# Optimization experiments

Hardware: AMD Instinct MI355X
Metric: run time of the kernel (lower is better)

The kernel has to match this reference:

```python
import jax, jax.numpy as jnp
import numpy as np

DIM_SINGLE = 384
DIM_PAIR = 128
HEADS = 12
DIM_POINT = 4
B, N = 1, 1024
EPS = 1e-5


def _gram_schmidt_rot(key, shape):
    k1, k2 = jax.random.split(key)
    v1 = jax.random.normal(k1, shape + (3,), jnp.float32)
    v2 = jax.random.normal(k2, shape + (3,), jnp.float32)
    x = v1 / jnp.linalg.norm(v1, axis=-1, keepdims=True)
    z = jnp.cross(x, v2)
    z = z / jnp.linalg.norm(z, axis=-1, keepdims=True)
    y = jnp.cross(z, x)
    # columns are basis vectors, matching torch.stack([x,y,z], dim=-1)
    return jnp.stack([x, y, z], axis=-1)


def setup_inputs() -> dict:
    key = jax.random.key(0)
    ks = jax.random.split(key, 24)
    C, Cp, H, P = DIM_SINGLE, DIM_PAIR, HEADS, DIM_POINT
    HP3 = H * P * 3
    s = lambda k, sh, sc: (jax.random.normal(k, sh, jnp.float32) * sc)
    inp = {
        'single': jax.random.normal(ks[0], (B, N, C), jnp.float32),
        'pair': jax.random.normal(ks[1], (B, N, N, Cp), jnp.float32),
        'rot': _gram_schmidt_rot(ks[2], (B, N)),
        'trans': jax.random.normal(ks[3], (B, N, 3), jnp.float32),
        'mask': jnp.ones((B, N), dtype=bool),
        'Wq': s(ks[4], (C, C), C ** -0.5), 'bq': jnp.zeros((C,), jnp.float32),
        'Wk': s(ks[5], (C, C), C ** -0.5), 'bk': jnp.zeros((C,), jnp.float32),
        'Wv': s(ks[6], (C, C), C ** -0.5), 'bv': jnp.zeros((C,), jnp.float32),
        'Wpb': s(ks[7], (Cp, H), Cp ** -0.5), 'bpb': jnp.zeros((H,), jnp.float32),
        'Wqp': s(ks[8], (C, HP3), C ** -0.5), 'bqp': jnp.zeros((HP3,), jnp.float32),
        'Wkp': s(ks[9], (C, HP3), C ** -0.5), 'bkp': jnp.zeros((HP3,), jnp.float32),
        'Wvp': s(ks[10], (C, HP3), C ** -0.5), 'bvp': jnp.zeros((HP3,), jnp.float32),
        'Wo': s(ks[11], (C, C), C ** -0.5), 'bo': jnp.zeros((C,), jnp.float32),
        'Wpo': s(ks[12], (HP3, C), HP3 ** -0.5), 'bpo': jnp.zeros((C,), jnp.float32),
        'gamma': jnp.ones((C,), jnp.float32), 'beta': jnp.zeros((C,), jnp.float32),
    }
    return inp


def ipa_forward(single, pair, rot, trans, mask,
                Wq, bq, Wk, bk, Wv, bv, Wpb, bpb,
                Wqp, bqp, Wkp, bkp, Wvp, bvp,
                Wo, bo, Wpo, bpo, gamma, beta):
    Bn, Nn, C = single.shape
    H, P = HEADS, DIM_POINT
    Ch = C // H
    scale = Ch ** -0.5

    q = (single @ Wq + bq).reshape(Bn, Nn, H, Ch)
    k = (single @ Wk + bk).reshape(Bn, Nn, H, Ch)
    v = (single @ Wv + bv).reshape(Bn, Nn, H, Ch)

    pair_bias = (pair @ Wpb + bpb).transpose(0, 3, 1, 2)  # [B,H,N,N]

    def pts(W, b):
        p = (single @ W + b).reshape(Bn, Nn, H, P, 3)
        # point as row-vector times rot (matches torch einsum bnhpd,bnhde->bnhpe)
        p = jnp.einsum('bnhpd,bnde->bnhpe', p, rot) + trans[:, :, None, None, :]
        return p

    q_pts = pts(Wqp, bqp)
    k_pts = pts(Wkp, bkp)
    v_pts = pts(Wvp, bvp)

    q2 = jnp.sum(q_pts ** 2, axis=(3, 4))  # [B,N,H]
    k2 = jnp.sum(k_pts ** 2, axis=(3, 4))

    scalar_logits = jnp.einsum('bmhc,bnhc->bhmn', q, k) * scale
    qk_pts = jnp.einsum('bmhpd,bnhpd->bhmn', q_pts, k_pts)
    point_logits = -0.5 * (q2.transpose(0, 2, 1)[:, :, :, None]
                           + k2.transpose(0, 2, 1)[:, :, None, :]
                           - 2.0 * qk_pts) * scale
    logits = scalar_logits + point_logits + pair_bias

    mask2d = mask[:, None, :, None] & mask[:, None, None, :]  # [B,1,M,N]
    logits = jnp.where(mask2d, logits, -1e9)

    attn = jax.nn.softmax(logits, axis=-1)  # [B,H,M,N]

    out_scalar = jnp.einsum('bhmn,bnhc->bmhc', attn, v).reshape(Bn, Nn, C)
    out_points = jnp.einsum('bhmn,bnhpd->bmhpd', attn, v_pts).reshape(Bn, Nn, H * P * 3)

    out = out_scalar @ Wo + bo + out_points @ Wpo + bpo
    x = single + out
    mu = jnp.mean(x, axis=-1, keepdims=True)
    var = jnp.var(x, axis=-1, keepdims=True)
    return (x - mu) / jnp.sqrt(var + EPS) * gamma + beta


def reference(single, pair, rot, trans, mask,
              Wq, bq, Wk, bk, Wv, bv, Wpb, bpb,
              Wqp, bqp, Wkp, bkp, Wvp, bvp,
              Wo, bo, Wpo, bpo, gamma, beta):
    return ipa_forward(single, pair, rot, trans, mask,
                       Wq, bq, Wk, bk, Wv, bv, Wpb, bpb,
                       Wqp, bqp, Wkp, bkp, Wvp, bvp,
                       Wo, bo, Wpo, bpo, gamma, beta)
```

## Files before the change

### kernel.cpp

```cpp
#include <hip/hip_runtime.h>
#include <cmath>


#define SCALE 0.17677669529663687f

#define OFF_QQ 0u
#define OFF_KK 589824u
#define OFF_VV 1179648u
#define OFF_SM 1769472u
#define OFF_SIS 1781760u
#define OFF_OA4 1794048u
#define OFF_OA 3956736u
#define OFF_LG 4497408u
#define OFF_TMP 17080320u
#define WS_FLOATS 18702336ull

__device__ __forceinline__ void fma4(float4& a, const float4& w, float s) {
  a.x = fmaf(w.x, s, a.x); a.y = fmaf(w.y, s, a.y);
  a.z = fmaf(w.z, s, a.z); a.w = fmaf(w.w, s, a.w);
}

__global__ __launch_bounds__(256) void k_gemm(
    const float* __restrict__ single,
    const float* __restrict__ Wq, const float* __restrict__ bq,
    const float* __restrict__ Wk, const float* __restrict__ bk,
    const float* __restrict__ Wv, const float* __restrict__ bv,
    const float* __restrict__ Wqp, const float* __restrict__ bqp,
    const float* __restrict__ Wkp, const float* __restrict__ bkp,
    const float* __restrict__ Wvp, const float* __restrict__ bvp,
    float* __restrict__ TMP)
{
  __shared__ float sA[64 * 37];
  __shared__ float sB[48 * 37];
  const int tid = threadIdx.x;
  const int m0 = blockIdx.x * 64;
  const int ct = blockIdx.y;
  const float* W; const float* bb; int OUT, cb;
  if (ct < 24) {
    int w_ = ct >> 3;
    W  = w_ == 0 ? Wq : (w_ == 1 ? Wk : Wv);
    bb = w_ == 0 ? bq : (w_ == 1 ? bk : bv);
    OUT = 384; cb = (ct & 7) * 48;
  } else {
    int pt = ct - 24; int w_ = pt / 3;
    W  = w_ == 0 ? Wqp : (w_ == 1 ? Wkp : Wvp);
    bb = w_ == 0 ? bqp : (w_ == 1 ? bkp : bvp);
    OUT = 144; cb = (pt - w_ * 3) * 48;
  }
  const int tr = tid >> 4, tc = tid & 15;
  const int r0 = tr * 4;
  const int k4s = tid & 7, mrs = tid >> 3;
  const int c4b = tid % 12, kkb = tid / 12;
  const int f1 = tid + 256;
  const int c4b1 = f1 % 12, kkb1 = f1 / 12;

  float acc[4][3];
  #pragma unroll
  for (int i = 0; i < 4; ++i)
    #pragma unroll
    for (int j = 0; j < 3; ++j) acc[i][j] = 0.f;

  float4 pa0 = *(const float4*)&single[(size_t)(m0 + mrs) * 384 + k4s * 4];
  float4 pa1 = *(const float4*)&single[(size_t)(m0 + mrs + 32) * 384 + k4s * 4];
  float4 pb0 = *(const float4*)&W[(size_t)kkb * OUT + cb + c4b * 4];
  float4 pb1;
  if (tid < 128) pb1 = *(const float4*)&W[(size_t)kkb1 * OUT + cb + c4b1 * 4];

  for (int kc = 0; kc < 12; ++kc) {
    *(float4*)&sA[mrs * 37 + k4s * 4] = pa0;
    *(float4*)&sA[(mrs + 32) * 37 + k4s * 4] = pa1;
    sB[(c4b * 4 + 0) * 37 + kkb] = pb0.x;
    sB[(c4b * 4 + 1) * 37 + kkb] = pb0.y;
    sB[(c4b * 4 + 2) * 37 + kkb] = pb0.z;
    sB[(c4b * 4 + 3) * 37 + kkb] = pb0.w;
    if (tid < 128) {
      sB[(c4b1 * 4 + 0) * 37 + kkb1] = pb1.x;
      sB[(c4b1 * 4 + 1) * 37 + kkb1] = pb1.y;
      sB[(c4b1 * 4 + 2) * 37 + kkb1] = pb1.z;
      sB[(c4b1 * 4 + 3) * 37 + kkb1] = pb1.w;
    }
    if (kc < 11) {
      int kn = (kc + 1) * 32;
      pa0 = *(const float4*)&single[(size_t)(m0 + mrs) * 384 + kn + k4s * 4];
      pa1 = *(const float4*)&single[(size_t)(m0 + mrs + 32) * 384 + kn + k4s * 4];
      pb0 = *(const float4*)&W[(size_t)(kn + kkb) * OUT + cb + c4b * 4];
      if (tid < 128) pb1 = *(const float4*)&W[(size_t)(kn + kkb1) * OUT + cb + c4b1 * 4];
    }
    __syncthreads();
    #pragma unroll
    for (int k4 = 0; k4 < 8; ++k4) {
      float4 av[4], bv_[3];
      #pragma unroll
      for (int i = 0; i < 4; ++i) av[i] = *(const float4*)&sA[(r0 + i) * 37 + k4 * 4];
      #pragma unroll
      for (int j = 0; j < 3; ++j) bv_[j] = *(const float4*)&sB[(tc * 3 + j) * 37 + k4 * 4];
      #pragma unroll
      for (int i = 0; i < 4; ++i)
        #pragma unroll
        for (int j = 0; j < 3; ++j)
          acc[i][j] += av[i].x * bv_[j].x + av[i].y * bv_[j].y
                     + av[i].z * bv_[j].z + av[i].w * bv_[j].w;
    }
    __syncthreads();
  }
  #pragma unroll
  for (int i = 0; i < 4; ++i)
    #pragma unroll
    for (int j = 0; j < 3; ++j) {
      int c = tc * 3 + j;
      TMP[(size_t)(m0 + r0 + i) * 1584 + ct * 48 + c] = acc[i][j] + bb[cb + c];
    }
}

__global__ __launch_bounds__(256) void k_epi(
    const float* __restrict__ TMP, const float* __restrict__ rotm,
    const float* __restrict__ trans, const float* __restrict__ bpb,
    float* __restrict__ ws)
{
  __shared__ float srot[288];
  const int tid = threadIdx.x;
  const int m = blockIdx.x;
  const float* t = TMP + (size_t)m * 1584;
  float* QQ = ws + OFF_QQ; float* KK = ws + OFF_KK; float* VV = ws + OFF_VV;

  for (int i = tid; i < 1152; i += 256) {
    int seg = i / 384, idx = i - seg * 384;
    int h = idx >> 5, c = idx & 31;
    float val = t[i];
    if (seg == 0)      QQ[h * 49152 + m * 48 + c] = SCALE * val;
    else if (seg == 1) KK[h * 49152 + m * 48 + c] = val;
    else               VV[m * 576 + h * 48 + c] = val;
  }
  const float* R = rotm + m * 9;
  for (int i = tid; i < 432; i += 256) {
    int seg = i / 144, r = i - seg * 144;
    int h = r / 12, pe = r - h * 12, p = pe / 3, e = pe - p * 3;
    const float* raw = t + 1152 + seg * 144 + h * 12 + p * 3;
    float val = raw[0] * R[e] + raw[1] * R[3 + e] + raw[2] * R[6 + e] + trans[m * 3 + e];
    if (seg == 0)      { srot[r] = val;       QQ[h * 49152 + m * 48 + 32 + pe] = SCALE * val; }
    else if (seg == 1) { srot[144 + r] = val; KK[h * 49152 + m * 48 + 32 + pe] = val; }
    else               VV[m * 576 + h * 48 + 32 + pe] = val;
  }
  __syncthreads();
  if (tid < 24) {
    int seg = tid / 12, h = tid - seg * 12;
    float s2 = 0.f;
    #pragma unroll
    for (int j = 0; j < 12; ++j) {
      float x = srot[seg * 144 + h * 12 + j];
      s2 = fmaf(x, x, s2);
    }
    if (seg == 0) {
      float* d = QQ + h * 49152 + m * 48;
      d[44] = 1.f; d[45] = -0.5f * SCALE * s2; d[46] = 0.f; d[47] = 0.f;
    } else {
      float* d = KK + h * 49152 + m * 48;
      d[44] = bpb[h] - 0.5f * SCALE * s2; d[45] = 1.f; d[46] = 0.f; d[47] = 0.f;
    }
  }
}

__global__ __launch_bounds__(256) void k_qkdot(const float* __restrict__ QQ,
                                               const float* __restrict__ KK,
                                               float* __restrict__ LG)
{
  __shared__ float sQ[64 * 52];
  __shared__ float sK[128 * 52];
  const int tid = threadIdx.x;
  const int n0 = blockIdx.x * 128, m0 = blockIdx.y * 64, hh = blockIdx.z;
  const float* Qg = QQ + (size_t)hh * 49152 + (size_t)m0 * 48;
  const float* Kg = KK + (size_t)hh * 49152 + (size_t)n0 * 48;
  for (int i = tid; i < 768; i += 256) {
    int r = i / 12, c4 = (i - r * 12) * 4;
    *(float4*)&sQ[r * 52 + c4] = *(const float4*)&Qg[r * 48 + c4];
  }
  for (int i = tid; i < 1536; i += 256) {
    int r = i / 12, c4 = (i - r * 12) * 4;
    *(float4*)&sK[r * 52 + c4] = *(const float4*)&Kg[r * 48 + c4];
  }
  __syncthreads();
  const int mb = (tid >> 4) * 4, nb = tid & 15;
  float acc[4][8];
  #pragma unroll
  for (int i = 0; i < 4; ++i)
    #pragma unroll
    for (int j = 0; j < 8; ++j) acc[i][j] = 0.f;
  #pragma unroll
  for (int j4 = 0; j4 < 48; j4 += 4) {
    float4 q[4], k[8];
    #pragma unroll
    for (int i = 0; i < 4; ++i) q[i] = *(const float4*)&sQ[(mb + i) * 52 + j4];
    #pragma unroll
    for (int j = 0; j < 8; ++j) k[j] = *(const float4*)&sK[(nb + j * 16) * 52 + j4];
    #pragma unroll
    for (int i = 0; i < 4; ++i)
      #pragma unroll
      for (int j = 0; j < 8; ++j)
        acc[i][j] += q[i].x * k[j].x + q[i].y * k[j].y + q[i].z * k[j].z + q[i].w * k[j].w;
  }
  float* Lb = LG + (size_t)hh * 1048576 + (size_t)m0 * 1024 + n0;
  #pragma unroll
  for (int i = 0; i < 4; ++i)
    #pragma unroll
    for (int j = 0; j < 8; ++j)
      Lb[(mb + i) * 1024 + nb + j * 16] = acc[i][j];
}

__global__ __launch_bounds__(256) void k_bias(const float* __restrict__ pair,
                                              const float* __restrict__ Wpb,
                                              float* __restrict__ LG)
{
  __shared__ float sP[256 * 33];
  const int tid = threadIdx.x;
  const size_t base = (size_t)blockIdx.x * 256;
  const int c4 = tid & 7, r8 = tid >> 3;
  float acc[12];
  #pragma unroll
  for (int h = 0; h < 12; ++h) acc[h] = 0.f;

  float4 pre[8];
  #pragma unroll
  for (int k = 0; k < 8; ++k)
    pre[k] = *(const float4*)&pair[(base + k * 32 + r8) * 128 + c4 * 4];

  for (int cc = 0; cc < 4; ++cc) {
    #pragma unroll
    for (int k = 0; k < 8; ++k) {
      float* d = &sP[(k * 32 + r8) * 33 + c4 * 4];
      d[0] = pre[k].x; d[1] = pre[k].y; d[2] = pre[k].z; d[3] = pre[k].w;
    }
    if (cc < 3) {
      #pragma unroll
      for (int k = 0; k < 8; ++k)
        pre[k] = *(const float4*)&pair[(base + k * 32 + r8) * 128 + (cc + 1) * 32 + c4 * 4];
    }
    __syncthreads();
    const float* rp = &sP[tid * 33];
    #pragma unroll 8
    for (int j = 0; j < 32; ++j) {
      float p = rp[j];
      const float* w = Wpb + (cc * 32 + j) * 12;
      #pragma unroll
      for (int h = 0; h < 12; ++h) acc[h] = fmaf(p, w[h], acc[h]);
    }
    __syncthreads();
  }
  float* L = LG + base + tid;
  #pragma unroll
  for (int h = 0; h < 12; ++h) L[(size_t)h * 1048576] += acc[h];
}

__global__ __launch_bounds__(256) void k_stats(const float* __restrict__ LG,
                                               float* __restrict__ SM,
                                               float* __restrict__ SIS)
{
  const int tid = threadIdx.x;
  const int m0 = blockIdx.x * 16, hh = blockIdx.y;
  const int lane = tid & 63, wv = tid >> 6;
  const float* Lh = LG + (size_t)hh * 1048576;
  #pragma unroll
  for (int rr = 0; rr < 4; ++rr) {
    int r = m0 + wv * 4 + rr;
    float m = -3.0e38f, s = 0.f;
    #pragma unroll
    for (int ch = 0; ch < 4; ++ch) {
      float4 x = *(const float4*)&Lh[(size_t)r * 1024 + ch * 256 + lane * 4];
      float mx = fmaxf(fmaxf(x.x, x.y), fmaxf(x.z, x.w));
      #pragma unroll
      for (int d = 32; d; d >>= 1) mx = fmaxf(mx, __shfl_xor(mx, d));
      float mn = fmaxf(m, mx);
      float sum = __expf(x.x - mn) + __expf(x.y - mn)
                + __expf(x.z - mn) + __expf(x.w - mn);
      #pragma unroll
      for (int d = 32; d; d >>= 1) sum += __shfl_xor(sum, d);
      s = s * __expf(m - mn) + sum;
      m = mn;
    }
    if (lane == 0) {
      SM[hh * 1024 + r] = m;
      SIS[hh * 1024 + r] = 1.f / s;
    }
  }
}

__global__ __launch_bounds__(256) void k_av(const float* __restrict__ LG,
                                            const float* __restrict__ VV,
                                            const float* __restrict__ SM,
                                            float* __restrict__ OA4)
{
  __shared__ float sA[64 * 68];
  __shared__ float sBt[48 * 68];
  __shared__ float sMl[64];
  const int tid = threadIdx.x;
  const int m0 = blockIdx.x * 64, n0 = blockIdx.y * 256, hh = blockIdx.z;
  const int q = blockIdx.y;
  const float* Lh = LG + (size_t)hh * 1048576;
  const int mi4 = tid >> 4, cj3 = tid & 15;

  if (tid < 64) sMl[tid] = SM[hh * 1024 + m0 + tid];
  for (int i = tid; i < 4 * 68; i += 256) sBt[44 * 68 + i] = 0.f;
  __syncthreads();

  float acc[4][3];
  #pragma unroll
  for (int i = 0; i < 4; ++i)
    #pragma unroll
    for (int j = 0; j < 3; ++j) acc[i][j] = 0.f;

  for (int kc = 0; kc < 4; ++kc) {
    const int nb = n0 + kc * 64;
    #pragma unroll
    for (int t = 0; t < 4; ++t) {
      int idx = tid + t * 256;
      int row = idx >> 4, c4 = idx & 15;
      float4 x = *(const float4*)&Lh[(size_t)(m0 + row) * 1024 + nb + c4 * 4];
      float mrow = sMl[row];
      float4 e;
      e.x = __expf(x.x - mrow); e.y = __expf(x.y - mrow);
      e.z = __expf(x.z - mrow); e.w = __expf(x.w - mrow);
      *(float4*)&sA[row * 68 + c4 * 4] = e;
    }
    for (int idx = tid; idx < 704; idx += 256) {
      int r = idx / 11, c4 = idx - r * 11;
      float4 v = *(const float4*)&VV[(size_t)(nb + r) * 576 + hh * 48 + c4 * 4];
      sBt[(c4 * 4 + 0) * 68 + r] = v.x;
      sBt[(c4 * 4 + 1) * 68 + r] = v.y;
      sBt[(c4 * 4 + 2) * 68 + r] = v.z;
      sBt[(c4 * 4 + 3) * 68 + r] = v.w;
    }
    __syncthreads();
    #pragma unroll 4
    for (int k4 = 0; k4 < 16; ++k4) {
      float4 a0 = *(const float4*)&sA[(mi4 * 4 + 0) * 68 + k4 * 4];
      float4 a1 = *(const float4*)&sA[(mi4 * 4 + 1) * 68 + k4 * 4];
      float4 a2 = *(const float4*)&sA[(mi4 * 4 + 2) * 68 + k4 * 4];
      float4 a3 = *(const float4*)&sA[(mi4 * 4 + 3) * 68 + k4 * 4];
      float4 b0 = *(const float4*)&sBt[(cj3 * 3 + 0) * 68 + k4 * 4];
      float4 b1 = *(const float4*)&sBt[(cj3 * 3 + 1) * 68 + k4 * 4];
      float4 b2 = *(const float4*)&sBt[(cj3 * 3 + 2) * 68 + k4 * 4];
      acc[0][0] += a0.x*b0.x + a0.y*b0.y + a0.z*b0.z + a0.w*b0.w;
      acc[0][1] += a0.x*b1.x + a0.y*b1.y + a0.z*b1.z + a0.w*b1.w;
      acc[0][2] += a0.x*b2.x + a0.y*b2.y + a0.z*b2.z + a0.w*b2.w;
      acc[1][0] += a1.x*b0.x + a1.y*b0.y + a1.z*b0.z + a1.w*b0.w;
      acc[1][1] += a1.x*b1.x + a1.y*b1.y + a1.z*b1.z + a1.w*b1.w;
      acc[1][2] += a1.x*b2.x + a1.y*b2.y + a1.z*b2.z + a1.w*b2.w;
      acc[2][0] += a2.x*b0.x + a2.y*b0.y + a2.z*b0.z + a2.w*b0.w;
      acc[2][1] += a2.x*b1.x + a2.y*b1.y + a2.z*b1.z + a2.w*b1.w;
      acc[2][2] += a2.x*b2.x + a2.y*b2.y + a2.z*b2.z + a2.w*b2.w;
      acc[3][0] += a3.x*b0.x + a3.y*b0.y + a3.z*b0.z + a3.w*b0.w;
      acc[3][1] += a3.x*b1.x + a3.y*b1.y + a3.z*b1.z + a3.w*b1.w;
      acc[3][2] += a3.x*b2.x + a3.y*b2.y + a3.z*b2.z + a3.w*b2.w;
    }
    __syncthreads();
  }
  #pragma unroll
  for (int i = 0; i < 4; ++i)
    #pragma unroll
    for (int j = 0; j < 3; ++j) {
      int c = cj3 * 3 + j;
      if (c < 44)
        OA4[(size_t)q * 540672 + (size_t)(m0 + mi4 * 4 + i) * 528 + hh * 44 + c]
            = acc[i][j];
    }
}

__global__ __launch_bounds__(256) void k_merge(const float* __restrict__ OA4,
                                               const float* __restrict__ SIS,
                                               float* __restrict__ OA)
{
  int idx = blockIdx.x * 256 + threadIdx.x;
  if (idx >= 540672) return;
  int m = idx / 528, c = idx - m * 528;
  int h = c / 44;
  float v = OA4[idx] + OA4[540672 + idx] + OA4[2 * 540672 + idx]
          + OA4[3 * 540672 + idx];
  OA[idx] = v * SIS[h * 1024 + m];
}

__global__ __launch_bounds__(128) void k_final(
    const float* __restrict__ OA, const float* __restrict__ single,
    const float* __restrict__ Wo, const float* __restrict__ bo,
    const float* __restrict__ Wpo, const float* __restrict__ bpo,
    const float* __restrict__ gamma, const float* __restrict__ beta,
    float* __restrict__ out)
{
  __shared__ float sX[2 * 384];
  const int tid = threadIdx.x;
  const int m0 = blockIdx.x * 2;
  if (tid < 96) {
    int o4 = tid * 4;
    float4 b1 = *(const float4*)&bo[o4];
    float4 b2 = *(const float4*)&bpo[o4];
    float4 bs = make_float4(b1.x + b2.x, b1.y + b2.y, b1.z + b2.z, b1.w + b2.w);
    float4 acc[2] = {bs, bs};
    const float* oab = OA + (size_t)m0 * 528;
    #pragma unroll 1
    for (int hh = 0; hh < 12; ++hh) {
      #pragma unroll
      for (int j4 = 0; j4 < 8; ++j4) {
        const float* wp = Wo + (size_t)(hh * 32 + j4 * 4) * 384 + o4;
        float4 w0 = *(const float4*)(wp);
        float4 w1 = *(const float4*)(wp + 384);
        float4 w2 = *(const float4*)(wp + 768);
        float4 w3 = *(const float4*)(wp + 1152);
        #pragma unroll
        for (int mi = 0; mi < 2; ++mi) {
          float4 s = *(const float4*)(oab + mi * 528 + hh * 44 + j4 * 4);
          fma4(acc[mi], w0, s.x); fma4(acc[mi], w1, s.y);
          fma4(acc[mi], w2, s.z); fma4(acc[mi], w3, s.w);
        }
      }
      #pragma unroll
      for (int j4 = 0; j4 < 3; ++j4) {
        const float* wp = Wpo + (size_t)(hh * 12 + j4 * 4) * 384 + o4;
        float4 w0 = *(const float4*)(wp);
        float4 w1 = *(const float4*)(wp + 384);
        float4 w2 = *(const float4*)(wp + 768);
        float4 w3 = *(const float4*)(wp + 1152);
        #pragma unroll
        for (int mi = 0; mi < 2; ++mi) {
          float4 s = *(const float4*)(oab + mi * 528 + hh * 44 + 32 + j4 * 4);
          fma4(acc[mi], w0, s.x); fma4(acc[mi], w1, s.y);
          fma4(acc[mi], w2, s.z); fma4(acc[mi], w3, s.w);
        }
      }
    }
    #pragma unroll
    for (int mi = 0; mi < 2; ++mi) {
      float4 sg = *(const float4*)&single[(size_t)(m0 + mi) * 384 + o4];
      float4 x = make_float4(acc[mi].x + sg.x, acc[mi].y + sg.y,
                             acc[mi].z + sg.z, acc[mi].w + sg.w);
      *(float4*)&sX[mi * 384 + o4] = x;
    }
  }
  __syncthreads();
  const int lane = tid & 63, r = tid >> 6;
  float xs[6]; float s = 0.f;
  #pragma unroll
  for (int i = 0; i < 6; ++i) { xs[i] = sX[r * 384 + lane * 6 + i]; s += xs[i]; }
  #pragma unroll
  for (int d = 32; d; d >>= 1) s += __shfl_xor(s, d);
  float mu = s * (1.f / 384.f);
  float vs = 0.f;
  #pragma unroll
  for (int i = 0; i < 6; ++i) { float dd = xs[i] - mu; vs = fmaf(dd, dd, vs); }
  #pragma unroll
  for (int d = 32; d; d >>= 1) vs += __shfl_xor(vs, d);
  float rstd = rsqrtf(vs * (1.f / 384.f) + 1e-5f);
  #pragma unroll
  for (int i = 0; i < 6; ++i) {
    int c = lane * 6 + i;
    out[(size_t)(m0 + r) * 384 + c] = (xs[i] - mu) * rstd * gamma[c] + beta[c];
  }
}

__global__ void k_wsfail(float* out, int n) {
  int i = blockIdx.x * 256 + threadIdx.x;
  if (i < n) out[i] = 12345.0f;
}

extern "C" void kernel_launch(void* const* d_in, const int* in_sizes, int n_in,
                              void* d_out, int out_size, void* d_ws, size_t ws_size,
                              hipStream_t stream)
{
  (void)in_sizes; (void)n_in;
  const float* single = (const float*)d_in[0];
  const float* pair   = (const float*)d_in[1];
  const float* rotm   = (const float*)d_in[2];
  const float* trans  = (const float*)d_in[3];
  const float* Wq  = (const float*)d_in[5];
  const float* bq  = (const float*)d_in[6];
  const float* Wk  = (const float*)d_in[7];
  const float* bk  = (const float*)d_in[8];
  const float* Wv  = (const float*)d_in[9];
  const float* bv  = (const float*)d_in[10];
  const float* Wpb = (const float*)d_in[11];
  const float* bpb = (const float*)d_in[12];
  const float* Wqp = (const float*)d_in[13];
  const float* bqp = (const float*)d_in[14];
  const float* Wkp = (const float*)d_in[15];
  const float* bkp = (const float*)d_in[16];
  const float* Wvp = (const float*)d_in[17];
  const float* bvp = (const float*)d_in[18];
  const float* Wo  = (const float*)d_in[19];
  const float* bo  = (const float*)d_in[20];
  const float* Wpo = (const float*)d_in[21];
  const float* bpo = (const float*)d_in[22];
  const float* gamma = (const float*)d_in[23];
  const float* beta  = (const float*)d_in[24];
  float* ws  = (float*)d_ws;
  float* out = (float*)d_out;

  if (ws_size < WS_FLOATS * 4ull) {
    k_wsfail<<<(out_size + 255) / 256, 256, 0, stream>>>(out, out_size);
    return;
  }

  k_gemm<<<dim3(16, 33), 256, 0, stream>>>(single,
      Wq, bq, Wk, bk, Wv, bv, Wqp, bqp, Wkp, bkp, Wvp, bvp, ws + OFF_TMP);
  k_epi<<<1024, 256, 0, stream>>>(ws + OFF_TMP, rotm, trans, bpb, ws);
  k_qkdot<<<dim3(8, 16, 12), 256, 0, stream>>>(ws + OFF_QQ, ws + OFF_KK,
                                               ws + OFF_LG);
  k_bias<<<4096, 256, 0, stream>>>(pair, Wpb, ws + OFF_LG);
  k_stats<<<dim3(64, 12), 256, 0, stream>>>(ws + OFF_LG, ws + OFF_SM,
                                            ws + OFF_SIS);
  k_av<<<dim3(16, 4, 12), 256, 0, stream>>>(ws + OFF_LG, ws + OFF_VV,
                                            ws + OFF_SM, ws + OFF_OA4);
  k_merge<<<2112, 256, 0, stream>>>(ws + OFF_OA4, ws + OFF_SIS, ws + OFF_OA);
  k_final<<<512, 128, 0, stream>>>(ws + OFF_OA, single, Wo, bo, Wpo, bpo,
                                   gamma, beta, out);
}
```

Before: 334.4 us.

## Fuse projection epilogue into GEMM and softmax stats into bias kernel

Moves the Q/K/V scatter, point rotation/translation and squared-norm terms into the projection GEMM epilogue, eliminating the TMP buffer and the separate epilogue kernel. Computes per-chunk row max and exp-sum inside the pair-bias kernel while the logits are in registers, then merges the four partials per row in a small kernel. This removes a full extra read pass over the logits tensor, at the cost of extra shuffles, shared-memory reductions and scattered stores in the fused kernels.

Measured after the change: 309.5 us (median of 3 runs). -7.4%, faster.

```diff
diff --git a/kernel.cpp b/kernel.cpp
--- a/kernel.cpp
+++ b/kernel.cpp
@@ -12,8 +12,9 @@
 #define OFF_OA4 1794048u
 #define OFF_OA 3956736u
 #define OFF_LG 4497408u
-#define OFF_TMP 17080320u
-#define WS_FLOATS 18702336ull
+#define OFF_PM 17080320u
+#define OFF_PS 17129472u
+#define WS_FLOATS 17178624ull
 
 __device__ __forceinline__ void fma4(float4& a, const float4& w, float s) {
   a.x = fmaf(w.x, s, a.x); a.y = fmaf(w.y, s, a.y);
@@ -21,28 +22,30 @@
 }
 
 __global__ __launch_bounds__(256) void k_gemm(
-    const float* __restrict__ single,
+    const float* __restrict__ single, const float* __restrict__ rotm,
+    const float* __restrict__ trans, const float* __restrict__ bpb,
     const float* __restrict__ Wq, const float* __restrict__ bq,
     const float* __restrict__ Wk, const float* __restrict__ bk,
     const float* __restrict__ Wv, const float* __restrict__ bv,
     const float* __restrict__ Wqp, const float* __restrict__ bqp,
     const float* __restrict__ Wkp, const float* __restrict__ bkp,
     const float* __restrict__ Wvp, const float* __restrict__ bvp,
-    float* __restrict__ TMP)
+    float* __restrict__ ws)
 {
   __shared__ float sA[64 * 37];
   __shared__ float sB[48 * 37];
   const int tid = threadIdx.x;
   const int m0 = blockIdx.x * 64;
   const int ct = blockIdx.y;
-  const float* W; const float* bb; int OUT, cb;
+  float* QQ = ws + OFF_QQ; float* KK = ws + OFF_KK; float* VV = ws + OFF_VV;
+  const float* W; const float* bb; int OUT, cb, w_;
   if (ct < 24) {
-    int w_ = ct >> 3;
+    w_ = ct >> 3;
     W  = w_ == 0 ? Wq : (w_ == 1 ? Wk : Wv);
     bb = w_ == 0 ? bq : (w_ == 1 ? bk : bv);
     OUT = 384; cb = (ct & 7) * 48;
   } else {
-    int pt = ct - 24; int w_ = pt / 3;
+    int pt = ct - 24; w_ = pt / 3;
     W  = w_ == 0 ? Wqp : (w_ == 1 ? Wkp : Wvp);
     bb = w_ == 0 ? bqp : (w_ == 1 ? bkp : bvp);
     OUT = 144; cb = (pt - w_ * 3) * 48;
@@ -103,59 +106,60 @@
     }
     __syncthreads();
   }
-  #pragma unroll
-  for (int i = 0; i < 4; ++i)
-    #pragma unroll
-    for (int j = 0; j < 3; ++j) {
-      int c = tc * 3 + j;
-      TMP[(size_t)(m0 + r0 + i) * 1584 + ct * 48 + c] = acc[i][j] + bb[cb + c];
-    }
-}
-
-__global__ __launch_bounds__(256) void k_epi(
-    const float* __restrict__ TMP, const float* __restrict__ rotm,
-    const float* __restrict__ trans, const float* __restrict__ bpb,
-    float* __restrict__ ws)
-{
-  __shared__ float srot[288];
-  const int tid = threadIdx.x;
-  const int m = blockIdx.x;
-  const float* t = TMP + (size_t)m * 1584;
-  float* QQ = ws + OFF_QQ; float* KK = ws + OFF_KK; float* VV = ws + OFF_VV;
-
-  for (int i = tid; i < 1152; i += 256) {
-    int seg = i / 384, idx = i - seg * 384;
-    int h = idx >> 5, c = idx & 31;
-    float val = t[i];
-    if (seg == 0)      QQ[h * 49152 + m * 48 + c] = SCALE * val;
-    else if (seg == 1) KK[h * 49152 + m * 48 + c] = val;
-    else               VV[m * 576 + h * 48 + c] = val;
-  }
-  const float* R = rotm + m * 9;
-  for (int i = tid; i < 432; i += 256) {
-    int seg = i / 144, r = i - seg * 144;
-    int h = r / 12, pe = r - h * 12, p = pe / 3, e = pe - p * 3;
-    const float* raw = t + 1152 + seg * 144 + h * 12 + p * 3;
-    float val = raw[0] * R[e] + raw[1] * R[3 + e] + raw[2] * R[6 + e] + trans[m * 3 + e];
-    if (seg == 0)      { srot[r] = val;       QQ[h * 49152 + m * 48 + 32 + pe] = SCALE * val; }
-    else if (seg == 1) { srot[144 + r] = val; KK[h * 49152 + m * 48 + 32 + pe] = val; }
-    else               VV[m * 576 + h * 48 + 32 + pe] = val;
-  }
-  __syncthreads();
-  if (tid < 24) {
-    int seg = tid / 12, h = tid - seg * 12;
-    float s2 = 0.f;
-    #pragma unroll
-    for (int j = 0; j < 12; ++j) {
-      float x = srot[seg * 144 + h * 12 + j];
-      s2 = fmaf(x, x, s2);
-    }
-    if (seg == 0) {
-      float* d = QQ + h * 49152 + m * 48;
-      d[44] = 1.f; d[45] = -0.5f * SCALE * s2; d[46] = 0.f; d[47] = 0.f;
-    } else {
-      float* d = KK + h * 49152 + m * 48;
-      d[44] = bpb[h] - 0.5f * SCALE * s2; d[45] = 1.f; d[46] = 0.f; d[47] = 0.f;
+
+  if (ct < 24) {
+    #pragma unroll
+    for (int i = 0; i < 4; ++i) {
+      int m = m0 + r0 + i;
+      #pragma unroll
+      for (int j = 0; j < 3; ++j) {
+        int c = cb + tc * 3 + j;
+        float v = acc[i][j] + bb[c];
+        int h = c >> 5, cc = c & 31;
+        if (w_ == 0)      QQ[h * 49152 + m * 48 + cc] = SCALE * v;
+        else if (w_ == 1) KK[h * 49152 + m * 48 + cc] = v;
+        else              VV[m * 576 + h * 48 + cc] = v;
+      }
+    }
+  } else {
+    const int pe = cb / 3 + tc;
+    const int h = pe >> 2, p = pe & 3;
+    #pragma unroll
+    for (int i = 0; i < 4; ++i) {
+      int m = m0 + r0 + i;
+      const float* R = rotm + m * 9;
+      float raw0 = acc[i][0] + bb[cb + tc * 3 + 0];
+      float raw1 = acc[i][1] + bb[cb + tc * 3 + 1];
+      float raw2 = acc[i][2] + bb[cb + tc * 3 + 2];
+      float v0 = raw0 * R[0] + raw1 * R[3] + raw2 * R[6] + trans[m * 3 + 0];
+      float v1 = raw0 * R[1] + raw1 * R[4] + raw2 * R[7] + trans[m * 3 + 1];
+      float v2 = raw0 * R[2] + raw1 * R[5] + raw2 * R[8] + trans[m * 3 + 2];
+      if (w_ == 2) {
+        float* d = VV + m * 576 + h * 48 + 32 + p * 3;
+        d[0] = v0; d[1] = v1; d[2] = v2;
+      } else {
+        float s2 = v0 * v0 + v1 * v1 + v2 * v2;
+        s2 += __shfl_xor(s2, 1);
+        s2 += __shfl_xor(s2, 2);
+        if (w_ == 0) {
+          float* d = QQ + h * 49152 + m * 48;
+          d[32 + p * 3 + 0] = SCALE * v0;
+          d[32 + p * 3 + 1] = SCALE * v1;
+          d[32 + p * 3 + 2] = SCALE * v2;
+          if (p == 0) {
+            d[44] = 1.f; d[45] = -0.5f * SCALE * s2; d[46] = 0.f; d[47] = 0.f;
+          }
+        } else {
+          float* d = KK + h * 49152 + m * 48;
+          d[32 + p * 3 + 0] = v0;
+          d[32 + p * 3 + 1] = v1;
+          d[32 + p * 3 + 2] = v2;
+          if (p == 0) {
+            d[44] = bpb[h] - 0.5f * SCALE * s2; d[45] = 1.f;
+            d[46] = 0.f; d[47] = 0.f;
+          }
+        }
+      }
     }
   }
 }
@@ -208,9 +212,13 @@
 
 __global__ __launch_bounds__(256) void k_bias(const float* __restrict__ pair,
                                               const float* __restrict__ Wpb,
-                                              float* __restrict__ LG)
+                                              float* __restrict__ LG,
+                                              float* __restrict__ PM,
+                                              float* __restrict__ PS)
 {
   __shared__ float sP[256 * 33];
+  __shared__ float sRed[4][12];
+  __shared__ float sRed2[4][12];
   const int tid = threadIdx.x;
   const size_t base = (size_t)blockIdx.x * 256;
   const int c4 = tid & 7, r8 = tid >> 3;
@@ -245,42 +253,56 @@
     }
     __syncthreads();
   }
+  float lf[12];
   float* L = LG + base + tid;
   #pragma unroll
-  for (int h = 0; h < 12; ++h) L[(size_t)h * 1048576] += acc[h];
-}
-
-__global__ __launch_bounds__(256) void k_stats(const float* __restrict__ LG,
-                                               float* __restrict__ SM,
-                                               float* __restrict__ SIS)
-{
-  const int tid = threadIdx.x;
-  const int m0 = blockIdx.x * 16, hh = blockIdx.y;
+  for (int h = 0; h < 12; ++h) {
+    lf[h] = L[(size_t)h * 1048576] + acc[h];
+    L[(size_t)h * 1048576] = lf[h];
+  }
   const int lane = tid & 63, wv = tid >> 6;
-  const float* Lh = LG + (size_t)hh * 1048576;
-  #pragma unroll
-  for (int rr = 0; rr < 4; ++rr) {
-    int r = m0 + wv * 4 + rr;
-    float m = -3.0e38f, s = 0.f;
-    #pragma unroll
-    for (int ch = 0; ch < 4; ++ch) {
-      float4 x = *(const float4*)&Lh[(size_t)r * 1024 + ch * 256 + lane * 4];
-      float mx = fmaxf(fmaxf(x.x, x.y), fmaxf(x.z, x.w));
-      #pragma unroll
-      for (int d = 32; d; d >>= 1) mx = fmaxf(mx, __shfl_xor(mx, d));
-      float mn = fmaxf(m, mx);
-      float sum = __expf(x.x - mn) + __expf(x.y - mn)
-                + __expf(x.z - mn) + __expf(x.w - mn);
-      #pragma unroll
-      for (int d = 32; d; d >>= 1) sum += __shfl_xor(sum, d);
-      s = s * __expf(m - mn) + sum;
-      m = mn;
-    }
-    if (lane == 0) {
-      SM[hh * 1024 + r] = m;
-      SIS[hh * 1024 + r] = 1.f / s;
-    }
-  }
+  #pragma unroll
+  for (int h = 0; h < 12; ++h) {
+    float mx = lf[h];
+    #pragma unroll
+    for (int d = 32; d; d >>= 1) mx = fmaxf(mx, __shfl_xor(mx, d));
+    if (lane == 0) sRed[wv][h] = mx;
+  }
+  __syncthreads();
+  float Mq[12];
+  #pragma unroll
+  for (int h = 0; h < 12; ++h)
+    Mq[h] = fmaxf(fmaxf(sRed[0][h], sRed[1][h]), fmaxf(sRed[2][h], sRed[3][h]));
+  #pragma unroll
+  for (int h = 0; h < 12; ++h) {
+    float se = __expf(lf[h] - Mq[h]);
+    #pragma unroll
+    for (int d = 32; d; d >>= 1) se += __shfl_xor(se, d);
+    if (lane == 0) sRed2[wv][h] = se;
+  }
+  __syncthreads();
+  if (tid < 12) {
+    float S = sRed2[0][tid] + sRed2[1][tid] + sRed2[2][tid] + sRed2[3][tid];
+    int m = blockIdx.x >> 2, q = blockIdx.x & 3;
+    PM[tid * 4096 + m * 4 + q] = Mq[tid];
+    PS[tid * 4096 + m * 4 + q] = S;
+  }
+}
+
+__global__ __launch_bounds__(256) void k_mstats(const float* __restrict__ PM,
+                                                const float* __restrict__ PS,
+                                                float* __restrict__ SM,
+                                                float* __restrict__ SIS)
+{
+  int idx = blockIdx.x * 256 + threadIdx.x;
+  if (idx >= 12288) return;
+  int b = idx * 4;
+  float m0 = PM[b], m1 = PM[b + 1], m2 = PM[b + 2], m3 = PM[b + 3];
+  float M = fmaxf(fmaxf(m0, m1), fmaxf(m2, m3));
+  float S = PS[b] * __expf(m0 - M) + PS[b + 1] * __expf(m1 - M)
+          + PS[b + 2] * __expf(m2 - M) + PS[b + 3] * __expf(m3 - M);
+  SM[idx] = M;
+  SIS[idx] = 1.f / S;
 }
 
 __global__ __launch_bounds__(256) void k_av(const float* __restrict__ LG,
@@ -496,14 +518,14 @@
     return;
   }
 
-  k_gemm<<<dim3(16, 33), 256, 0, stream>>>(single,
-      Wq, bq, Wk, bk, Wv, bv, Wqp, bqp, Wkp, bkp, Wvp, bvp, ws + OFF_TMP);
-  k_epi<<<1024, 256, 0, stream>>>(ws + OFF_TMP, rotm, trans, bpb, ws);
+  k_gemm<<<dim3(16, 33), 256, 0, stream>>>(single, rotm, trans, bpb,
+      Wq, bq, Wk, bk, Wv, bv, Wqp, bqp, Wkp, bkp, Wvp, bvp, ws);
   k_qkdot<<<dim3(8, 16, 12), 256, 0, stream>>>(ws + OFF_QQ, ws + OFF_KK,
                                                ws + OFF_LG);
-  k_bias<<<4096, 256, 0, stream>>>(pair, Wpb, ws + OFF_LG);
-  k_stats<<<dim3(64, 12), 256, 0, stream>>>(ws + OFF_LG, ws + OFF_SM,
-                                            ws + OFF_SIS);
+  k_bias<<<4096, 256, 0, stream>>>(pair, Wpb, ws + OFF_LG, ws + OFF_PM,
+                                   ws + OFF_PS);
+  k_mstats<<<48, 256, 0, stream>>>(ws + OFF_PM, ws + OFF_PS, ws + OFF_SM,
+                                   ws + OFF_SIS);
   k_av<<<dim3(16, 4, 12), 256, 0, stream>>>(ws + OFF_LG, ws + OFF_VV,
                                             ws + OFF_SM, ws + OFF_OA4);
   k_merge<<<2112, 256, 0, stream>>>(ws + OFF_OA4, ws + OFF_SIS, ws + OFF_OA);
```
